# Kernel tuning notes

Hardware: AMD Instinct MI355X
Metric: run time of the kernel (lower is better)

Reference implementation:

```python
import jax, jax.numpy as jnp
import numpy as np


def _sigmax_weights(score, hlens):
    # score: [B,T] (treated as a constant / detached, as in the torch code),
    # hlens: [B] int. Returns detached weight_cmat [B,T,M] and hlens_new [B].
    B, T = score.shape
    left = jnp.concatenate([score[:, :1], score[:, :-1]], axis=1)
    right = jnp.concatenate([score[:, 1:], score[:, -1:]], axis=1)
    valleys = (score >= left) & (score >= right)
    valleys = valleys.at[:, 0].set(True)
    valleys = valleys.at[jnp.arange(B), hlens - 1].set(True)
    frame_ok = jnp.arange(T)[None, :] < hlens[:, None]
    v = valleys & frame_ok                       # valleys within valid length
    hlens_new = v.sum(axis=1).astype(jnp.int32)  # segments per utterance
    M = int(jnp.max(hlens_new))                  # concrete (eager) max_len
    # scatter valley frame indices into a padded [B, M] table (ragged -> dense)
    rank = jnp.cumsum(v, axis=1) - 1
    tgt = jnp.where(v, rank, M)                  # non-valleys go to dummy col M
    frames = jnp.broadcast_to(jnp.arange(T, dtype=jnp.int32)[None, :], (B, T))
    vi = jnp.zeros((B, M + 1), dtype=jnp.int32)
    vi = vi.at[jnp.arange(B)[:, None], tgt].set(frames)[:, :M]
    # segment k covers frames [vstart[k], vend[k]) per the torch slicing
    vstart = jnp.concatenate([jnp.zeros((B, 1), jnp.int32), vi[:, :-1]], axis=1)
    k_idx = jnp.arange(M)[None, :]
    vend_shift = jnp.concatenate([vi[:, 1:], jnp.zeros((B, 1), jnp.int32)], axis=1)
    vend = jnp.where(k_idx == hlens_new[:, None] - 1,
                     (hlens - 1)[:, None].astype(jnp.int32), vend_shift)
    seg_valid = k_idx < hlens_new[:, None]
    # per-segment score sums via exclusive prefix sums
    csum = jnp.concatenate([jnp.zeros((B, 1), score.dtype), jnp.cumsum(score, axis=1)], axis=1)
    segsum = jnp.take_along_axis(csum, vend, axis=1) - jnp.take_along_axis(csum, vstart, axis=1)
    f = jnp.arange(T)
    member = (f[None, :, None] >= vstart[:, None, :]) & \
             (f[None, :, None] < vend[:, None, :]) & seg_valid[:, None, :]
    weight_cmat = member.astype(score.dtype) / (segsum[:, None, :] + 1e-10)
    return weight_cmat, hlens_new


def setup_inputs() -> dict:
    key = jax.random.key(0)
    k1, k2, k3, k4 = jax.random.split(key, 4)
    B, T, D = 16, 2000, 512
    feat = jax.random.normal(k1, (B, T, D), dtype=jnp.float32)
    W = jax.random.normal(k2, (D,), dtype=jnp.float32) / np.sqrt(D)
    b = jax.random.normal(k3, (1,), dtype=jnp.float32)
    hlens = jax.random.randint(k4, (B,), T // 2, T + 1).astype(jnp.int32)
    return {"feat": feat, "W": W, "b": b, "hlens": hlens}


def reference(feat, W, b, hlens):
    # score = Sigmoid(Linear(feat)) -> [B,T]
    score = jax.nn.sigmoid(jnp.einsum('btd,d->bt', feat, W) + b)
    weight_cmat, hlens_new = _sigmax_weights(jax.lax.stop_gradient(score), hlens)
    weight_mat = score[:, :, None] * weight_cmat            # [B,T,M]
    # feat^T @ weight_mat, transposed back -> [B,M,D]
    feat_new = jnp.einsum('btd,btk->bkd', feat, weight_mat)
    return feat_new, hlens_new, score
```

## Files before the change

kernel.cpp:

```cpp
#include <hip/hip_runtime.h>
#include <math.h>

#define MAX_T 2048
#define SEG_P 4

__global__ void score_kernel(const float* __restrict__ feat,
                             const float* __restrict__ W,
                             const float* __restrict__ bias,
                             float* __restrict__ score,
                             int nrows, int D) {
  int row = blockIdx.x * 4 + (threadIdx.x >> 6);
  int lane = threadIdx.x & 63;
  if (row >= nrows) return;
  const float4* f4 = (const float4*)(feat + (size_t)row * D);
  const float4* w4 = (const float4*)W;
  float acc = 0.f;
  int n4 = D >> 2;
  for (int idx = lane; idx < n4; idx += 64) {
    float4 a = f4[idx];
    float4 w = w4[idx];
    acc += a.x * w.x + a.y * w.y + a.z * w.z + a.w * w.w;
  }
#pragma unroll
  for (int off = 32; off > 0; off >>= 1) acc += __shfl_xor(acc, off, 64);
  if (lane == 0) {
    float x = acc + bias[0];
    score[row] = 1.f / (1.f + expf(-x));
  }
}

__global__ void seg_kernel(const float* __restrict__ score,
                           const int* __restrict__ hlens,
                           int* __restrict__ vi_ws,
                           int* __restrict__ hn_ws,
                           float* __restrict__ hn_out,
                           int T, int M) {
  int b = blockIdx.x;
  int tid = threadIdx.x;
  __shared__ float s[MAX_T];
  __shared__ unsigned char fl[MAX_T];
  __shared__ int vi[MAX_T];
  __shared__ int wsum[4];

  const float* sr = score + (size_t)b * T;
  int hl = hlens[b];

  for (int t = tid; t < T; t += 256) s[t] = sr[t];
  __syncthreads();

  for (int t = tid; t < T; t += 256) {
    bool f;
    if (t >= hl) {
      f = false;
    } else if (t == 0 || t == hl - 1) {
      f = true;
    } else {
      float c = s[t];
      f = (c >= s[t - 1]) && (c >= s[t + 1]);
    }
    fl[t] = f ? (unsigned char)1 : (unsigned char)0;
  }
  __syncthreads();

  int C = (T + 255) / 256;
  int lo = tid * C;
  int hi = lo + C; if (hi > T) hi = T; if (lo > T) lo = T;
  int cnt = 0;
  for (int t = lo; t < hi; ++t) cnt += fl[t];

  int lane = tid & 63, wid = tid >> 6;
  int incl = cnt;
#pragma unroll
  for (int off = 1; off < 64; off <<= 1) {
    int v = __shfl_up(incl, off, 64);
    if (lane >= off) incl += v;
  }
  if (lane == 63) wsum[wid] = incl;
  __syncthreads();
  int wofs = 0;
#pragma unroll
  for (int w = 0; w < 4; ++w) wofs += (w < wid) ? wsum[w] : 0;
  int hn = wsum[0] + wsum[1] + wsum[2] + wsum[3];
  int excl = wofs + incl - cnt;
  for (int t = lo; t < hi; ++t) {
    if (fl[t]) vi[excl++] = t;
  }
  __syncthreads();

  for (int j = tid; j < M; j += 256) {
    vi_ws[(size_t)b * M + j] = (j < hn) ? vi[j] : 0;
  }
  if (tid == 0) {
    hn_ws[b] = hn;
    hn_out[b] = (float)hn;
  }
}

__global__ __launch_bounds__(128) void pool_kernel(
    const float* __restrict__ feat, const float* __restrict__ score,
    const int* __restrict__ vi_ws, const int* __restrict__ hn_ws,
    float* __restrict__ out, int T, int D, int M, int ngrp) {
  int gid = blockIdx.x;
  int lane = threadIdx.x;
  int b = gid / ngrp;
  int g = gid - b * ngrp;
  int k0 = g * SEG_P;
  if (k0 >= M) return;

  int hn = hn_ws[b];
  const int* vi = vi_ws + (size_t)b * M;
  const float* sr = score + (size_t)b * T;
  const float4* fr = (const float4*)(feat + (size_t)b * T * (size_t)D);
  int n4 = D >> 2;

  int kend = k0 + SEG_P; if (kend > M) kend = M;

  float4 ap = make_float4(0.f, 0.f, 0.f, 0.f);
  float ssp = 0.f;
  if (k0 < hn) {
    int as = (k0 == 0) ? 0 : vi[k0 - 1];
    int ae = vi[k0];
    for (int t = as; t < ae; ++t) {
      float sc = sr[t];
      float4 f = fr[(size_t)t * n4 + lane];
      ap.x += sc * f.x; ap.y += sc * f.y; ap.z += sc * f.z; ap.w += sc * f.w;
      ssp += sc;
    }
  }

  for (int k = k0; k < kend; ++k) {
    float4* o4 = (float4*)(out + ((size_t)b * M + k) * D);
    if (k >= hn) {
      o4[lane] = make_float4(0.f, 0.f, 0.f, 0.f);
      continue;
    }
    if (k == hn - 1) {
      float inv = 1.f / (ssp + 1e-10f);
      o4[lane] = make_float4(ap.x * inv, ap.y * inv, ap.z * inv, ap.w * inv);
      ssp = 0.f; ap = make_float4(0.f, 0.f, 0.f, 0.f);
      continue;
    }
    float4 ac = make_float4(0.f, 0.f, 0.f, 0.f);
    float ssc = 0.f;
    int as = vi[k];
    int ae = vi[k + 1];
    for (int t = as; t < ae; ++t) {
      float sc = sr[t];
      float4 f = fr[(size_t)t * n4 + lane];
      ac.x += sc * f.x; ac.y += sc * f.y; ac.z += sc * f.z; ac.w += sc * f.w;
      ssc += sc;
    }
    float inv = 1.f / (ssp + ssc + 1e-10f);
    o4[lane] = make_float4((ap.x + ac.x) * inv, (ap.y + ac.y) * inv,
                           (ap.z + ac.z) * inv, (ap.w + ac.w) * inv);
    ap = ac; ssp = ssc;
  }
}

extern "C" void kernel_launch(void* const* d_in, const int* in_sizes, int n_in,
                              void* d_out, int out_size, void* d_ws, size_t ws_size,
                              hipStream_t stream) {
  const float* feat = (const float*)d_in[0];
  const float* W    = (const float*)d_in[1];
  const float* bias = (const float*)d_in[2];
  const int* hlens  = (const int*)d_in[3];

  int D = in_sizes[1];
  int B = in_sizes[3];
  int T = in_sizes[0] / (B * D);
  int M = (out_size - B - B * T) / (B * D);

  float* out      = (float*)d_out;
  float* hn_out   = out + (size_t)B * M * D;
  float* score    = hn_out + B;

  int* vi_ws = (int*)d_ws;
  int* hn_ws = vi_ws + (size_t)B * M;

  int nrows = B * T;
  score_kernel<<<(nrows + 3) / 4, 256, 0, stream>>>(feat, W, bias, score, nrows, D);
  seg_kernel<<<B, 256, 0, stream>>>(score, hlens, vi_ws, hn_ws, hn_out, T, M);

  int ngrp = (M + SEG_P - 1) / SEG_P;
  pool_kernel<<<B * ngrp, 128, 0, stream>>>(feat, score, vi_ws, hn_ws,
                                            out, T, D, M, ngrp);
}
```

Before: 35.29 us.

## Stream pool over a single frame span with prefetch; widen segment scan block

The pool kernel now walks one contiguous frame span covering all segments of its group. It keeps a one-row register prefetch of the next feature row, emits outputs at segment boundaries, and writes them with nontemporal stores. Padding rows are zeroed up front with an early exit. The segment-scan kernel moves from 256 to 1024 threads to shorten its serial per-thread loops. The pool loop hardcodes the row stride as 128 float4s (D=512), and its loop logic is more intricate.

Result: slower. 48.52 us (+37.5%).

```diff
diff --git a/kernel.cpp b/kernel.cpp
--- a/kernel.cpp
+++ b/kernel.cpp
@@ -3,6 +3,8 @@
 
 #define MAX_T 2048
 #define SEG_P 4
+
+typedef float f32x4 __attribute__((ext_vector_type(4)));
 
 __global__ void score_kernel(const float* __restrict__ feat,
                              const float* __restrict__ W,
@@ -29,32 +31,29 @@
   }
 }
 
-__global__ void seg_kernel(const float* __restrict__ score,
-                           const int* __restrict__ hlens,
-                           int* __restrict__ vi_ws,
-                           int* __restrict__ hn_ws,
-                           float* __restrict__ hn_out,
-                           int T, int M) {
+__global__ __launch_bounds__(1024) void seg_kernel(
+    const float* __restrict__ score, const int* __restrict__ hlens,
+    int* __restrict__ vi_ws, int* __restrict__ hn_ws,
+    float* __restrict__ hn_out, int T, int M) {
   int b = blockIdx.x;
   int tid = threadIdx.x;
+  const int NT = 1024;
   __shared__ float s[MAX_T];
   __shared__ unsigned char fl[MAX_T];
   __shared__ int vi[MAX_T];
-  __shared__ int wsum[4];
+  __shared__ int wsum[16];
 
   const float* sr = score + (size_t)b * T;
   int hl = hlens[b];
 
-  for (int t = tid; t < T; t += 256) s[t] = sr[t];
+  for (int t = tid; t < T; t += NT) s[t] = sr[t];
   __syncthreads();
 
-  for (int t = tid; t < T; t += 256) {
+  for (int t = tid; t < T; t += NT) {
     bool f;
-    if (t >= hl) {
-      f = false;
-    } else if (t == 0 || t == hl - 1) {
-      f = true;
-    } else {
+    if (t >= hl)                     f = false;
+    else if (t == 0 || t == hl - 1)  f = true;
+    else {
       float c = s[t];
       f = (c >= s[t - 1]) && (c >= s[t + 1]);
     }
@@ -62,7 +61,7 @@
   }
   __syncthreads();
 
-  int C = (T + 255) / 256;
+  int C = (T + NT - 1) / NT;
   int lo = tid * C;
   int hi = lo + C; if (hi > T) hi = T; if (lo > T) lo = T;
   int cnt = 0;
@@ -77,17 +76,19 @@
   }
   if (lane == 63) wsum[wid] = incl;
   __syncthreads();
-  int wofs = 0;
+  int wofs = 0, hn = 0;
 #pragma unroll
-  for (int w = 0; w < 4; ++w) wofs += (w < wid) ? wsum[w] : 0;
-  int hn = wsum[0] + wsum[1] + wsum[2] + wsum[3];
+  for (int w = 0; w < 16; ++w) {
+    if (w < wid) wofs += wsum[w];
+    hn += wsum[w];
+  }
   int excl = wofs + incl - cnt;
   for (int t = lo; t < hi; ++t) {
     if (fl[t]) vi[excl++] = t;
   }
   __syncthreads();
 
-  for (int j = tid; j < M; j += 256) {
+  for (int j = tid; j < M; j += NT) {
     vi_ws[(size_t)b * M + j] = (j < hn) ? vi[j] : 0;
   }
   if (tid == 0) {
@@ -106,55 +107,66 @@
   int g = gid - b * ngrp;
   int k0 = g * SEG_P;
   if (k0 >= M) return;
+  int kend = k0 + SEG_P; if (kend > M) kend = M;
 
   int hn = hn_ws[b];
+  int klast = kend < hn ? kend : hn;
+
+  for (int k = klast; k < kend; ++k) {
+    f32x4 z = (f32x4)(0.f);
+    __builtin_nontemporal_store(z, (f32x4*)(out + ((size_t)b * M + k) * D) + lane);
+  }
+  if (k0 >= hn) return;
+
   const int* vi = vi_ws + (size_t)b * M;
   const float* sr = score + (size_t)b * T;
   const float4* fr = (const float4*)(feat + (size_t)b * T * (size_t)D);
-  int n4 = D >> 2;
 
-  int kend = k0 + SEG_P; if (kend > M) kend = M;
+  int a_lo = k0;
+  int a_hi = klast < (hn - 1) ? klast : (hn - 1);
+  int span_s = (a_lo == 0) ? 0 : vi[a_lo - 1];
+  int span_e = vi[a_hi];
 
   float4 ap = make_float4(0.f, 0.f, 0.f, 0.f);
   float ssp = 0.f;
-  if (k0 < hn) {
-    int as = (k0 == 0) ? 0 : vi[k0 - 1];
-    int ae = vi[k0];
-    for (int t = as; t < ae; ++t) {
-      float sc = sr[t];
-      float4 f = fr[(size_t)t * n4 + lane];
-      ap.x += sc * f.x; ap.y += sc * f.y; ap.z += sc * f.z; ap.w += sc * f.w;
-      ssp += sc;
+  float4 cur = make_float4(0.f, 0.f, 0.f, 0.f);
+  float scur = 0.f;
+
+  auto emit = [&](int k, float nx, float ny, float nz, float nw, float den) {
+    float inv = 1.f / (den + 1e-10f);
+    f32x4 r;
+    r.x = nx * inv; r.y = ny * inv; r.z = nz * inv; r.w = nw * inv;
+    __builtin_nontemporal_store(r, (f32x4*)(out + ((size_t)b * M + k) * D) + lane);
+  };
+  auto complete = [&](int j) {
+    if (j > a_lo) {
+      int k = j - 1;
+      if (k < klast && k < hn - 1)
+        emit(k, ap.x + cur.x, ap.y + cur.y, ap.z + cur.z, ap.w + cur.w,
+             ssp + scur);
     }
+    if (j == hn - 1 && j >= k0 && j < klast)
+      emit(j, cur.x, cur.y, cur.z, cur.w, scur);
+    ap = cur; ssp = scur;
+  };
+
+  int j = a_lo;
+  int nextb = vi[j];
+  float4 fnext = (span_s < span_e) ? fr[(size_t)span_s * 128 + lane]
+                                   : make_float4(0.f, 0.f, 0.f, 0.f);
+  for (int t = span_s; t < span_e; ++t) {
+    while (t == nextb) {
+      complete(j);
+      ++j; nextb = vi[j];
+      cur = make_float4(0.f, 0.f, 0.f, 0.f); scur = 0.f;
+    }
+    float4 f = fnext;
+    if (t + 1 < span_e) fnext = fr[(size_t)(t + 1) * 128 + lane];
+    float sc = sr[t];
+    cur.x += sc * f.x; cur.y += sc * f.y; cur.z += sc * f.z; cur.w += sc * f.w;
+    scur += sc;
   }
-
-  for (int k = k0; k < kend; ++k) {
-    float4* o4 = (float4*)(out + ((size_t)b * M + k) * D);
-    if (k >= hn) {
-      o4[lane] = make_float4(0.f, 0.f, 0.f, 0.f);
-      continue;
-    }
-    if (k == hn - 1) {
-      float inv = 1.f / (ssp + 1e-10f);
-      o4[lane] = make_float4(ap.x * inv, ap.y * inv, ap.z * inv, ap.w * inv);
-      ssp = 0.f; ap = make_float4(0.f, 0.f, 0.f, 0.f);
-      continue;
-    }
-    float4 ac = make_float4(0.f, 0.f, 0.f, 0.f);
-    float ssc = 0.f;
-    int as = vi[k];
-    int ae = vi[k + 1];
-    for (int t = as; t < ae; ++t) {
-      float sc = sr[t];
-      float4 f = fr[(size_t)t * n4 + lane];
-      ac.x += sc * f.x; ac.y += sc * f.y; ac.z += sc * f.z; ac.w += sc * f.w;
-      ssc += sc;
-    }
-    float inv = 1.f / (ssp + ssc + 1e-10f);
-    o4[lane] = make_float4((ap.x + ac.x) * inv, (ap.y + ac.y) * inv,
-                           (ap.z + ac.z) * inv, (ap.w + ac.w) * inv);
-    ap = ac; ssp = ssc;
-  }
+  complete(a_hi);
 }
 
 extern "C" void kernel_launch(void* const* d_in, const int* in_sizes, int n_in,
@@ -179,7 +191,7 @@
 
   int nrows = B * T;
   score_kernel<<<(nrows + 3) / 4, 256, 0, stream>>>(feat, W, bias, score, nrows, D);
-  seg_kernel<<<B, 256, 0, stream>>>(score, hlens, vi_ws, hn_ws, hn_out, T, M);
+  seg_kernel<<<B, 1024, 0, stream>>>(score, hlens, vi_ws, hn_ws, hn_out, T, M);
 
   int ngrp = (M + SEG_P - 1) / SEG_P;
   pool_kernel<<<B * ngrp, 128, 0, stream>>>(feat, score, vi_ws, hn_ws,
```

## Fuse valley segmentation into pooling kernel, recomputing per block

Applied to the files above, without the earlier changes.

Removes the separate per-batch segmentation kernel and its workspace round-trip. Each pooling block now loads its row's scores into shared memory, finds the valleys, prefix-scans them, builds the valley index table in shared memory, and then pools. It also reads scores from shared memory instead of global. The cost is that every block redoes the segmentation scan for its batch row, and D=512 is now hardcoded through the row stride of 128 float4.

Result: slower. 48.97 us (+38.8%).

```diff
diff --git a/kernel.cpp b/kernel.cpp
--- a/kernel.cpp
+++ b/kernel.cpp
@@ -29,44 +29,37 @@
   }
 }
 
-__global__ void seg_kernel(const float* __restrict__ score,
-                           const int* __restrict__ hlens,
-                           int* __restrict__ vi_ws,
-                           int* __restrict__ hn_ws,
-                           float* __restrict__ hn_out,
-                           int T, int M) {
-  int b = blockIdx.x;
+__global__ __launch_bounds__(128) void segpool_kernel(
+    const float* __restrict__ feat, const float* __restrict__ score,
+    const int* __restrict__ hlens, float* __restrict__ out,
+    float* __restrict__ hn_out, int T, int D, int M, int ngrp) {
+  int gid = blockIdx.x;
   int tid = threadIdx.x;
+  int b = gid / ngrp;
+  int g = gid - b * ngrp;
+  int k0 = g * SEG_P;
+
   __shared__ float s[MAX_T];
-  __shared__ unsigned char fl[MAX_T];
-  __shared__ int vi[MAX_T];
-  __shared__ int wsum[4];
+  __shared__ unsigned short vi[MAX_T];
+  __shared__ int wsum[2];
 
   const float* sr = score + (size_t)b * T;
   int hl = hlens[b];
 
-  for (int t = tid; t < T; t += 256) s[t] = sr[t];
+  for (int t = tid; t < T; t += 128) s[t] = sr[t];
   __syncthreads();
 
-  for (int t = tid; t < T; t += 256) {
-    bool f;
-    if (t >= hl) {
-      f = false;
-    } else if (t == 0 || t == hl - 1) {
-      f = true;
-    } else {
-      float c = s[t];
-      f = (c >= s[t - 1]) && (c >= s[t + 1]);
-    }
-    fl[t] = f ? (unsigned char)1 : (unsigned char)0;
-  }
-  __syncthreads();
-
-  int C = (T + 255) / 256;
+  int C = (T + 127) / 128;
   int lo = tid * C;
   int hi = lo + C; if (hi > T) hi = T; if (lo > T) lo = T;
+  auto flag = [&](int t) -> bool {
+    if (t >= hl) return false;
+    if (t == 0 || t == hl - 1) return true;
+    float c = s[t];
+    return (c >= s[t - 1]) && (c >= s[t + 1]);
+  };
   int cnt = 0;
-  for (int t = lo; t < hi; ++t) cnt += fl[t];
+  for (int t = lo; t < hi; ++t) cnt += flag(t) ? 1 : 0;
 
   int lane = tid & 63, wid = tid >> 6;
   int incl = cnt;
@@ -77,43 +70,19 @@
   }
   if (lane == 63) wsum[wid] = incl;
   __syncthreads();
-  int wofs = 0;
-#pragma unroll
-  for (int w = 0; w < 4; ++w) wofs += (w < wid) ? wsum[w] : 0;
-  int hn = wsum[0] + wsum[1] + wsum[2] + wsum[3];
-  int excl = wofs + incl - cnt;
+  int hn = wsum[0] + wsum[1];
+  int excl = ((wid == 1) ? wsum[0] : 0) + incl - cnt;
   for (int t = lo; t < hi; ++t) {
-    if (fl[t]) vi[excl++] = t;
+    if (flag(t)) vi[excl++] = (unsigned short)t;
   }
   __syncthreads();
 
-  for (int j = tid; j < M; j += 256) {
-    vi_ws[(size_t)b * M + j] = (j < hn) ? vi[j] : 0;
-  }
-  if (tid == 0) {
-    hn_ws[b] = hn;
-    hn_out[b] = (float)hn;
-  }
-}
+  if (g == 0 && tid == 0) hn_out[b] = (float)hn;
+  if (k0 >= M) return;
+  int kend = k0 + SEG_P; if (kend > M) kend = M;
 
-__global__ __launch_bounds__(128) void pool_kernel(
-    const float* __restrict__ feat, const float* __restrict__ score,
-    const int* __restrict__ vi_ws, const int* __restrict__ hn_ws,
-    float* __restrict__ out, int T, int D, int M, int ngrp) {
-  int gid = blockIdx.x;
-  int lane = threadIdx.x;
-  int b = gid / ngrp;
-  int g = gid - b * ngrp;
-  int k0 = g * SEG_P;
-  if (k0 >= M) return;
-
-  int hn = hn_ws[b];
-  const int* vi = vi_ws + (size_t)b * M;
-  const float* sr = score + (size_t)b * T;
+  int lane4 = tid;
   const float4* fr = (const float4*)(feat + (size_t)b * T * (size_t)D);
-  int n4 = D >> 2;
-
-  int kend = k0 + SEG_P; if (kend > M) kend = M;
 
   float4 ap = make_float4(0.f, 0.f, 0.f, 0.f);
   float ssp = 0.f;
@@ -121,8 +90,8 @@
     int as = (k0 == 0) ? 0 : vi[k0 - 1];
     int ae = vi[k0];
     for (int t = as; t < ae; ++t) {
-      float sc = sr[t];
-      float4 f = fr[(size_t)t * n4 + lane];
+      float sc = s[t];
+      float4 f = fr[(size_t)t * 128 + lane4];
       ap.x += sc * f.x; ap.y += sc * f.y; ap.z += sc * f.z; ap.w += sc * f.w;
       ssp += sc;
     }
@@ -131,12 +100,12 @@
   for (int k = k0; k < kend; ++k) {
     float4* o4 = (float4*)(out + ((size_t)b * M + k) * D);
     if (k >= hn) {
-      o4[lane] = make_float4(0.f, 0.f, 0.f, 0.f);
+      o4[lane4] = make_float4(0.f, 0.f, 0.f, 0.f);
       continue;
     }
     if (k == hn - 1) {
       float inv = 1.f / (ssp + 1e-10f);
-      o4[lane] = make_float4(ap.x * inv, ap.y * inv, ap.z * inv, ap.w * inv);
+      o4[lane4] = make_float4(ap.x * inv, ap.y * inv, ap.z * inv, ap.w * inv);
       ssp = 0.f; ap = make_float4(0.f, 0.f, 0.f, 0.f);
       continue;
     }
@@ -145,14 +114,14 @@
     int as = vi[k];
     int ae = vi[k + 1];
     for (int t = as; t < ae; ++t) {
-      float sc = sr[t];
-      float4 f = fr[(size_t)t * n4 + lane];
+      float sc = s[t];
+      float4 f = fr[(size_t)t * 128 + lane4];
       ac.x += sc * f.x; ac.y += sc * f.y; ac.z += sc * f.z; ac.w += sc * f.w;
       ssc += sc;
     }
     float inv = 1.f / (ssp + ssc + 1e-10f);
-    o4[lane] = make_float4((ap.x + ac.x) * inv, (ap.y + ac.y) * inv,
-                           (ap.z + ac.z) * inv, (ap.w + ac.w) * inv);
+    o4[lane4] = make_float4((ap.x + ac.x) * inv, (ap.y + ac.y) * inv,
+                            (ap.z + ac.z) * inv, (ap.w + ac.w) * inv);
     ap = ac; ssp = ssc;
   }
 }
@@ -174,14 +143,10 @@
   float* hn_out   = out + (size_t)B * M * D;
   float* score    = hn_out + B;
 
-  int* vi_ws = (int*)d_ws;
-  int* hn_ws = vi_ws + (size_t)B * M;
-
   int nrows = B * T;
   score_kernel<<<(nrows + 3) / 4, 256, 0, stream>>>(feat, W, bias, score, nrows, D);
-  seg_kernel<<<B, 256, 0, stream>>>(score, hlens, vi_ws, hn_ws, hn_out, T, M);
 
   int ngrp = (M + SEG_P - 1) / SEG_P;
-  pool_kernel<<<B * ngrp, 128, 0, stream>>>(feat, score, vi_ws, hn_ws,
-                                            out, T, D, M, ngrp);
+  segpool_kernel<<<B * ngrp, 128, 0, stream>>>(feat, score, hlens, out, hn_out,
+                                               T, D, M, ngrp);
 }
```
